# Kernel optimization log

Measured on AMD Instinct MI355X. Metric: run time of the kernel, lower is better.

The kernel has to match this reference:

```python
import jax, jax.numpy as jnp
import numpy as np

N, F, D, H, OUT = 4096, 64, 64, 4, 2
NEG_SLOPE = 0.2


def setup_inputs() -> dict:
    key = jax.random.key(0)
    ks = jax.random.split(key, 16)
    def p(k, shape, fan):
        return jax.random.normal(k, shape, dtype=jnp.float32) / np.float32(np.sqrt(fan))
    return {
        "x": jax.random.normal(ks[0], (N, F), dtype=jnp.float32),
        "W_enc": p(ks[1], (F, D), F), "b_enc": jnp.zeros((D,), jnp.float32),
        "W1": p(ks[2], (D, H * D), D), "a_src1": p(ks[3], (H, D), D),
        "a_dst1": p(ks[4], (H, D), D), "b1": jnp.zeros((D,), jnp.float32),
        "W2": p(ks[5], (D, H * D), D), "a_src2": p(ks[6], (H, D), D),
        "a_dst2": p(ks[7], (H, D), D), "b2": jnp.zeros((D,), jnp.float32),
        "W_act": p(ks[8], (D, OUT), D), "b_act": jnp.zeros((OUT,), jnp.float32),
        "W_cri": p(ks[9], (D, 1), D), "b_cri": jnp.zeros((1,), jnp.float32),
    }


def gat_conv(x, W, a_src, a_dst, b):
    # PyG GATConv, fully-connected graph (incl. self loops), concat=False (mean heads)
    n = x.shape[0]
    h = (x @ W).reshape(n, H, D)                      # [N,H,D]
    s_src = jnp.einsum('nhd,hd->nh', h, a_src)        # alpha_src per source node
    s_dst = jnp.einsum('nhd,hd->nh', h, a_dst)        # alpha_dst per target node
    # e[t,s,h] = leaky_relu(alpha_dst[t] + alpha_src[s]); softmax over sources s
    e = jax.nn.leaky_relu(s_dst[:, None, :] + s_src[None, :, :], NEG_SLOPE)
    attn = jax.nn.softmax(e, axis=1)                  # [N,N,H]
    out = jnp.einsum('tsh,shd->thd', attn, h)         # aggregate messages
    return out.mean(axis=1) + b                       # head mean + bias -> [N,D]


def reference(x, W_enc, b_enc, W1, a_src1, a_dst1, b1, W2, a_src2, a_dst2, b2,
              W_act, b_act, W_cri, b_cri):
    h = jax.nn.relu(x @ W_enc + b_enc)
    h = jax.nn.relu(gat_conv(h, W1, a_src1, a_dst1, b1))
    h = jax.nn.relu(gat_conv(h, W2, a_src2, a_dst2, b2))
    logits = jnp.clip(h @ W_act + b_act, -5.0, 5.0)
    logits = jnp.concatenate([logits[:, :1], jnp.abs(logits[:, 1:2])], axis=1)
    values = (h @ W_cri + b_cri).reshape(-1)
    return logits, values
```

## Files before the change

kernel.cpp:

```cpp
#include <hip/hip_runtime.h>


#define N 4096
#define D 64
#define H 4
#define HD 256
#define TS 66

#define AS(p, v) __hip_atomic_store((p), (v), __ATOMIC_RELAXED, __HIP_MEMORY_SCOPE_AGENT)
#define AL(p)    __hip_atomic_load((p), __ATOMIC_RELAXED, __HIP_MEMORY_SCOPE_AGENT)

__device__ __forceinline__ void fma4(float4& a, float s, const float4& b) {
  a.x = fmaf(s, b.x, a.x); a.y = fmaf(s, b.y, a.y);
  a.z = fmaf(s, b.z, a.z); a.w = fmaf(s, b.w, a.w);
}

__device__ __forceinline__ void proj_dev(const float (*xs)[64], int r0,
    const float* __restrict__ W, const float* __restrict__ asrc,
    const float* __restrict__ adst, float* __restrict__ h2,
    float* __restrict__ ssrc, float* __restrict__ sdst) {
  int tid = threadIdx.x;
  int lane6 = tid & 63;
  int c0 = lane6 * 4;
  int hh = lane6 >> 4;
  int rbase = (tid >> 6) * 2;
  float4 acc0 = make_float4(0.f, 0.f, 0.f, 0.f);
  float4 acc1 = make_float4(0.f, 0.f, 0.f, 0.f);
#pragma unroll
  for (int kq = 0; kq < 16; ++kq) {
    const float* Wk = W + kq * 4 * 256 + c0;
    float4 w0 = *(const float4*)(Wk);
    float4 w1 = *(const float4*)(Wk + 256);
    float4 w2 = *(const float4*)(Wk + 512);
    float4 w3 = *(const float4*)(Wk + 768);
    float4 x0 = *(const float4*)(&xs[rbase][kq * 4]);
    float4 x1 = *(const float4*)(&xs[rbase + 1][kq * 4]);
    fma4(acc0, x0.x, w0); fma4(acc0, x0.y, w1); fma4(acc0, x0.z, w2); fma4(acc0, x0.w, w3);
    fma4(acc1, x1.x, w0); fma4(acc1, x1.y, w1); fma4(acc1, x1.z, w2); fma4(acc1, x1.w, w3);
  }
  float4 av = *(const float4*)(asrc + c0);
  float4 bv = *(const float4*)(adst + c0);
#pragma unroll
  for (int r = 0; r < 2; ++r) {
    float4 a = (r == 0) ? acc0 : acc1;
    int row = r0 + rbase + r;
    *(float4*)(h2 + row * 256 + c0) = a;
    float ps = a.x * av.x + a.y * av.y + a.z * av.z + a.w * av.w;
    float pd = a.x * bv.x + a.y * bv.y + a.z * bv.z + a.w * bv.w;
#pragma unroll
    for (int off = 8; off > 0; off >>= 1) {
      ps += __shfl_down(ps, off);
      pd += __shfl_down(pd, off);
    }
    if ((lane6 & 15) == 0) {
      ssrc[hh * N + row] = ps;
      sdst[hh * N + row] = pd;
    }
  }
}

__global__ __launch_bounds__(256) void k_encproj(const float* __restrict__ x,
    const float* __restrict__ Wenc, const float* __restrict__ benc,
    const float* __restrict__ W, const float* __restrict__ asrc,
    const float* __restrict__ adst, float* __restrict__ h2,
    float* __restrict__ ssrc, float* __restrict__ sdst,
    int* __restrict__ sync) {
  __shared__ float xs[8][64];
  int tid = threadIdx.x;
  int r0 = blockIdx.x * 8;
  if (blockIdx.x == 0 && tid < 136) sync[tid] = 0;
  {
    int row = tid >> 5, c = (tid & 31) * 2;
    const float* xr = x + (r0 + row) * 64;
    float a0 = benc[c], a1 = benc[c + 1];
#pragma unroll
    for (int k = 0; k < 64; ++k) {
      float xv = xr[k];
      float2 w = *(const float2*)(Wenc + k * 64 + c);
      a0 = fmaf(xv, w.x, a0);
      a1 = fmaf(xv, w.y, a1);
    }
    xs[row][c] = fmaxf(a0, 0.f);
    xs[row][c + 1] = fmaxf(a1, 0.f);
  }
  __syncthreads();
  proj_dev(xs, r0, W, asrc, adst, h2, ssrc, sdst);
}

__global__ __launch_bounds__(256) void k_rank_f(const float* __restrict__ ssrc,
    int* __restrict__ rpart, int* __restrict__ cnt,
    float* __restrict__ srtv, int* __restrict__ srti) {
  __shared__ __align__(16) float vs[256];
  __shared__ int lastflag;
  int h = blockIdx.x >> 4, ig = blockIdx.x & 15, c = blockIdx.y;
  int tid = threadIdx.x;
  vs[tid] = ssrc[h * N + c * 256 + tid];
  __syncthreads();
  int i = ig * 256 + tid;
  float vi = ssrc[h * N + i];
  int jbase = c * 256;
  int rank = 0;
  const float4* vs4 = (const float4*)vs;
#pragma unroll 4
  for (int j4 = 0; j4 < 64; ++j4) {
    float4 q = vs4[j4];
    int jb = jbase + (j4 << 2);
    rank += (q.x < vi || (q.x == vi && jb < i));
    rank += (q.y < vi || (q.y == vi && jb + 1 < i));
    rank += (q.z < vi || (q.z == vi && jb + 2 < i));
    rank += (q.w < vi || (q.w == vi && jb + 3 < i));
  }
  AS(&rpart[(c * H + h) * N + i], rank);
  asm volatile("s_waitcnt vmcnt(0)" ::: "memory");
  __syncthreads();
  if (tid == 0) {
    int prev = __hip_atomic_fetch_add(&cnt[h * 16 + ig], 1,
                 __ATOMIC_RELAXED, __HIP_MEMORY_SCOPE_AGENT);
    lastflag = (prev == 15);
  }
  __syncthreads();
  if (lastflag) {
    int rk = 0;
#pragma unroll
    for (int cc = 0; cc < 16; ++cc) rk += AL(&rpart[(cc * H + h) * N + i]);
    srtv[h * N + rk] = vi;
    srti[h * N + rk] = i;
  }
}

__global__ __launch_bounds__(512) void k_s3off(const float* __restrict__ h2,
    const int* __restrict__ srti, const float* __restrict__ srtv,
    float* __restrict__ TA, float* __restrict__ TB, int* __restrict__ cnt,
    float* __restrict__ SA, float* __restrict__ PB,
    float* __restrict__ SufT, float* __restrict__ PreT) {
  __shared__ int pj[64];
  __shared__ float wa[64], wb[64];
  __shared__ float vt[64][66];
  __shared__ float segA[8][66], segB[8][66];
  __shared__ int lastflag;
  int h = blockIdx.x >> 6, c = blockIdx.x & 63;
  int tid = threadIdx.x, w = tid >> 6, lane = tid & 63;
  int j0 = c * 64;
  if (tid < 64) {
    int j = j0 + tid;
    pj[tid] = srti[h * N + j];
    float sv = srtv[h * N + j];
    float m1 = srtv[h * N + N - 1];
    wa[tid] = expf(sv - m1);
    wb[tid] = expf(0.2f * (sv - m1));
  }
  __syncthreads();
#pragma unroll
  for (int jj = 0; jj < 8; ++jj) {
    int j = jj * 8 + w;
    vt[j][lane] = h2[pj[j] * HD + h * 64 + lane];
  }
  __syncthreads();
  {
    float sA = 0.f, sB = 0.f;
#pragma unroll
    for (int jj = 0; jj < 8; ++jj) {
      int j = w * 8 + jj;
      float v = vt[j][lane];
      sA = fmaf(wa[j], v, sA);
      sB = fmaf(wb[j], v, sB);
    }
    segA[w][lane] = sA; segB[w][lane] = sB;
    if (lane == 0) {
      float swA = 0.f, swB = 0.f;
#pragma unroll
      for (int jj = 0; jj < 8; ++jj) { swA += wa[w * 8 + jj]; swB += wb[w * 8 + jj]; }
      segA[w][64] = swA; segB[w][64] = swB;
    }
  }
  __syncthreads();
  size_t base = (size_t)h * (N + 1);
  {
    float acc = 0.f;
    for (int w2 = w + 1; w2 < 8; ++w2) acc += segA[w2][lane];
#pragma unroll
    for (int jj = 7; jj >= 0; --jj) {
      int j = w * 8 + jj;
      acc = fmaf(wa[j], vt[j][lane], acc);
      SA[(base + j0 + j) * TS + lane] = acc;
    }
  }
  {
    float acc = 0.f;
    for (int w2 = 0; w2 < w; ++w2) acc += segB[w2][lane];
#pragma unroll
    for (int jj = 0; jj < 8; ++jj) {
      int j = w * 8 + jj;
      PB[(base + j0 + j) * TS + lane] = acc;
      acc = fmaf(wb[j], vt[j][lane], acc);
    }
  }
  if (lane == 0) {
    float a = 0.f;
    for (int w2 = w + 1; w2 < 8; ++w2) a += segA[w2][64];
#pragma unroll
    for (int jj = 7; jj >= 0; --jj) {
      int j = w * 8 + jj;
      a += wa[j];
      SA[(base + j0 + j) * TS + 64] = a;
    }
  }
  if (lane == 1) {
    float bsum = 0.f;
    for (int w2 = 0; w2 < w; ++w2) bsum += segB[w2][64];
#pragma unroll
    for (int jj = 0; jj < 8; ++jj) {
      int j = w * 8 + jj;
      PB[(base + j0 + j) * TS + 64] = bsum;
      bsum += wb[j];
    }
  }
  if (tid < 65) {
    float tA = 0.f, tB = 0.f;
#pragma unroll
    for (int w2 = 0; w2 < 8; ++w2) { tA += segA[w2][tid]; tB += segB[w2][tid]; }
    AS(&TA[(h * 64 + c) * TS + tid], tA);
    AS(&TB[(h * 64 + c) * TS + tid], tB);
  }
  asm volatile("s_waitcnt vmcnt(0)" ::: "memory");
  __syncthreads();
  if (tid == 0) {
    int prev = __hip_atomic_fetch_add(&cnt[h], 1,
                 __ATOMIC_RELAXED, __HIP_MEMORY_SCOPE_AGENT);
    lastflag = (prev == 63);
  }
  __syncthreads();
  if (!lastflag) return;
  __syncthreads();
#pragma unroll
  for (int it = 0; it < 9; ++it) {
    int idx = it * 512 + tid;
    if (idx < 64 * 65) {
      int cc = idx / 65, col = idx - cc * 65;
      vt[cc][col] = AL(&TA[(h * 64 + cc) * TS + col]);
    }
  }
  __syncthreads();
  if (tid < 65) {
    float acc = 0.f;
    SufT[(h * 65 + 64) * TS + tid] = 0.f;
    for (int cc = 63; cc >= 0; --cc) {
      SufT[(h * 65 + cc) * TS + tid] = acc;
      acc += vt[cc][tid];
    }
  }
  __syncthreads();
#pragma unroll
  for (int it = 0; it < 9; ++it) {
    int idx = it * 512 + tid;
    if (idx < 64 * 65) {
      int cc = idx / 65, col = idx - cc * 65;
      vt[cc][col] = AL(&TB[(h * 64 + cc) * TS + col]);
    }
  }
  __syncthreads();
  if (tid < 65) {
    float acc = 0.f;
    for (int cc = 0; cc < 64; ++cc) {
      PreT[(h * 65 + cc) * TS + tid] = acc;
      acc += vt[cc][tid];
    }
    PreT[(h * 65 + 64) * TS + tid] = acc;
    SA[(base + N) * TS + tid] = 0.f;
    PB[(base + N) * TS + tid] = 0.f;
  }
}

template <int MODE>
__device__ __forceinline__ void target_dev(int t0, int tid,
    const float* __restrict__ sdst, const float* __restrict__ srtv,
    const float* __restrict__ SA, const float* __restrict__ PB,
    const float* __restrict__ SufT, const float* __restrict__ PreT,
    const float* __restrict__ bias, float (*xsout)[64], const float (*bnd)[64],
    const float* __restrict__ Wact, const float* __restrict__ bact,
    const float* __restrict__ Wcri, const float* __restrict__ bcri,
    float* __restrict__ out, int ntask) {
  int lane = tid & 63;
  for (int task = 0; task < ntask; ++task) {
    int r = task * 4 + (tid >> 6);
    int t = t0 + r;
    float acc = 0.f;
#pragma unroll
    for (int h = 0; h < H; ++h) {
      const float* sv = srtv + h * N;
      float dst = sdst[h * N + t];
      float thr = -dst;
      float m1 = sv[N - 1];
      unsigned long long b1m = __ballot(bnd[h][lane] <= thr);
      int c1 = __popcll(b1m);
      int seg = c1 > 0 ? c1 - 1 : 0;
      unsigned long long b2m = __ballot(sv[seg * 64 + lane] <= thr);
      int k = seg * 64 + __popcll(b2m);
      int c = k >> 6;
      float u = dst + m1;
      float g = fmaxf(u, 0.2f * u);
      float wAt = expf(u - g);
      float wBt = expf(0.2f * u - g);
      const float* sa = SA + (size_t)(h * (N + 1) + k) * TS;
      const float* pb = PB + (size_t)(h * (N + 1) + k) * TS;
      const float* sf = SufT + (size_t)(h * 65 + c) * TS;
      const float* pr = PreT + (size_t)(h * 65 + c) * TS;
      float num = wAt * (sa[lane] + sf[lane]) + wBt * (pb[lane] + pr[lane]);
      float den = wAt * (sa[64] + sf[64]) + wBt * (pb[64] + pr[64]);
      acc += num / den;
    }
    float hv = fmaxf(acc * 0.25f + bias[lane], 0.f);
    if constexpr (MODE == 0) {
      xsout[r][lane] = hv;
    } else {
      float p0 = hv * Wact[lane * 2 + 0];
      float p1 = hv * Wact[lane * 2 + 1];
      float p2 = hv * Wcri[lane];
#pragma unroll
      for (int off = 32; off > 0; off >>= 1) {
        p0 += __shfl_down(p0, off);
        p1 += __shfl_down(p1, off);
        p2 += __shfl_down(p2, off);
      }
      if (lane == 0) {
        float l0 = fminf(fmaxf(p0 + bact[0], -5.f), 5.f);
        float l1 = fminf(fmaxf(p1 + bact[1], -5.f), 5.f);
        out[t * 2 + 0] = l0;
        out[t * 2 + 1] = fabsf(l1);
        out[2 * N + t] = p2 + bcri[0];
      }
    }
  }
}

__global__ __launch_bounds__(256) void k_targetproj(
    const float* __restrict__ sdst, const float* __restrict__ srtv,
    const float* __restrict__ SA, const float* __restrict__ PB,
    const float* __restrict__ SufT, const float* __restrict__ PreT,
    const float* __restrict__ bias,
    const float* __restrict__ W, const float* __restrict__ asrc,
    const float* __restrict__ adst, float* __restrict__ h2,
    float* __restrict__ ssrc2, float* __restrict__ sdst2) {
  __shared__ float xs[8][64];
  __shared__ float bnd[4][64];
  int tid = threadIdx.x;
  int r0 = blockIdx.x * 8;
  { int hh = tid >> 6, l = tid & 63; bnd[hh][l] = srtv[hh * N + l * 64]; }
  __syncthreads();
  target_dev<0>(r0, tid, sdst, srtv, SA, PB, SufT, PreT, bias, xs, bnd,
                nullptr, nullptr, nullptr, nullptr, nullptr, 2);
  __syncthreads();
  proj_dev(xs, r0, W, asrc, adst, h2, ssrc2, sdst2);
}

__global__ __launch_bounds__(256) void k_target2(
    const float* __restrict__ sdst, const float* __restrict__ srtv,
    const float* __restrict__ SA, const float* __restrict__ PB,
    const float* __restrict__ SufT, const float* __restrict__ PreT,
    const float* __restrict__ bias,
    const float* __restrict__ Wact, const float* __restrict__ bact,
    const float* __restrict__ Wcri, const float* __restrict__ bcri,
    float* __restrict__ out) {
  __shared__ float bnd[4][64];
  int tid = threadIdx.x;
  { int hh = tid >> 6, l = tid & 63; bnd[hh][l] = srtv[hh * N + l * 64]; }
  __syncthreads();
  target_dev<1>(blockIdx.x * 4, tid, sdst, srtv, SA, PB, SufT, PreT, bias,
                nullptr, bnd, Wact, bact, Wcri, bcri, out, 1);
}

extern "C" void kernel_launch(void* const* d_in, const int* in_sizes, int n_in,
                              void* d_out, int out_size, void* d_ws, size_t ws_size,
                              hipStream_t stream) {
    (void)in_sizes; (void)n_in; (void)out_size; (void)ws_size;
    const float* x     = (const float*)d_in[0];
    const float* W_enc = (const float*)d_in[1];
    const float* b_enc = (const float*)d_in[2];
    const float* W1    = (const float*)d_in[3];
    const float* as1   = (const float*)d_in[4];
    const float* ad1   = (const float*)d_in[5];
    const float* b1    = (const float*)d_in[6];
    const float* W2    = (const float*)d_in[7];
    const float* as2   = (const float*)d_in[8];
    const float* ad2   = (const float*)d_in[9];
    const float* b2    = (const float*)d_in[10];
    const float* W_act = (const float*)d_in[11];
    const float* b_act = (const float*)d_in[12];
    const float* W_cri = (const float*)d_in[13];
    const float* b_cri = (const float*)d_in[14];
    float* out = (float*)d_out;

    float* p = (float*)d_ws;
    float* h2    = p; p += N * HD;
    float* ssrc1 = p; p += H * N;
    float* sdst1 = p; p += H * N;
    float* ssrc2 = p; p += H * N;
    float* sdst2 = p; p += H * N;
    float* srtv  = p; p += H * N;
    int*   srti  = (int*)p; p += H * N;
    float* TA    = p; p += H * 64 * TS;
    float* TB    = p; p += H * 64 * TS;
    float* SufT  = p; p += H * 65 * TS;
    float* PreT  = p; p += H * 65 * TS;
    float* SA    = p; p += (size_t)H * (N + 1) * TS;
    float* PB    = p; p += (size_t)H * (N + 1) * TS;
    int*   rpart = (int*)p; p += 16 * H * N;
    int*   sync  = (int*)p; p += 256;

    int* rcnt1 = sync;
    int* scnt1 = sync + 64;
    int* rcnt2 = sync + 68;
    int* scnt2 = sync + 132;

    dim3 rgrid(64, 16);

    k_encproj<<<N / 8, 256, 0, stream>>>(x, W_enc, b_enc, W1, as1, ad1,
                                         h2, ssrc1, sdst1, sync);
    k_rank_f<<<rgrid, 256, 0, stream>>>(ssrc1, rpart, rcnt1, srtv, srti);
    k_s3off<<<256, 512, 0, stream>>>(h2, srti, srtv, TA, TB, scnt1, SA, PB, SufT, PreT);
    k_targetproj<<<N / 8, 256, 0, stream>>>(sdst1, srtv, SA, PB, SufT, PreT, b1,
                                            W2, as2, ad2, h2, ssrc2, sdst2);
    k_rank_f<<<rgrid, 256, 0, stream>>>(ssrc2, rpart, rcnt2, srtv, srti);
    k_s3off<<<256, 512, 0, stream>>>(h2, srti, srtv, TA, TB, scnt2, SA, PB, SufT, PreT);
    k_target2<<<N / 4, 256, 0, stream>>>(sdst2, srtv, SA, PB, SufT, PreT, b2,
                                         W_act, b_act, W_cri, b_cri, out);
}
```

Baseline: 100.7 us.

## Fuse rank sort into scan kernel with per-head grid barrier

```diff
diff --git a/kernel.cpp b/kernel.cpp
--- a/kernel.cpp
+++ b/kernel.cpp
@@ -68,7 +68,7 @@
   __shared__ float xs[8][64];
   int tid = threadIdx.x;
   int r0 = blockIdx.x * 8;
-  if (blockIdx.x == 0 && tid < 136) sync[tid] = 0;
+  if (blockIdx.x == 0 && tid < 16) sync[tid] = 0;
   {
     int row = tid >> 5, c = (tid & 31) * 2;
     const float* xr = x + (r0 + row) * 64;
@@ -87,65 +87,70 @@
   proj_dev(xs, r0, W, asrc, adst, h2, ssrc, sdst);
 }
 
-__global__ __launch_bounds__(256) void k_rank_f(const float* __restrict__ ssrc,
-    int* __restrict__ rpart, int* __restrict__ cnt,
-    float* __restrict__ srtv, int* __restrict__ srti) {
-  __shared__ __align__(16) float vs[256];
-  __shared__ int lastflag;
-  int h = blockIdx.x >> 4, ig = blockIdx.x & 15, c = blockIdx.y;
-  int tid = threadIdx.x;
-  vs[tid] = ssrc[h * N + c * 256 + tid];
-  __syncthreads();
-  int i = ig * 256 + tid;
-  float vi = ssrc[h * N + i];
-  int jbase = c * 256;
-  int rank = 0;
-  const float4* vs4 = (const float4*)vs;
-#pragma unroll 4
-  for (int j4 = 0; j4 < 64; ++j4) {
-    float4 q = vs4[j4];
-    int jb = jbase + (j4 << 2);
-    rank += (q.x < vi || (q.x == vi && jb < i));
-    rank += (q.y < vi || (q.y == vi && jb + 1 < i));
-    rank += (q.z < vi || (q.z == vi && jb + 2 < i));
-    rank += (q.w < vi || (q.w == vi && jb + 3 < i));
-  }
-  AS(&rpart[(c * H + h) * N + i], rank);
-  asm volatile("s_waitcnt vmcnt(0)" ::: "memory");
-  __syncthreads();
-  if (tid == 0) {
-    int prev = __hip_atomic_fetch_add(&cnt[h * 16 + ig], 1,
-                 __ATOMIC_RELAXED, __HIP_MEMORY_SCOPE_AGENT);
-    lastflag = (prev == 15);
-  }
-  __syncthreads();
-  if (lastflag) {
-    int rk = 0;
-#pragma unroll
-    for (int cc = 0; cc < 16; ++cc) rk += AL(&rpart[(cc * H + h) * N + i]);
-    srtv[h * N + rk] = vi;
-    srti[h * N + rk] = i;
-  }
-}
-
-__global__ __launch_bounds__(512) void k_s3off(const float* __restrict__ h2,
-    const int* __restrict__ srti, const float* __restrict__ srtv,
-    float* __restrict__ TA, float* __restrict__ TB, int* __restrict__ cnt,
+__global__ __launch_bounds__(512) void k_rankscan(const float* __restrict__ ssrc,
+    float* __restrict__ srtv, int* __restrict__ srti, int* __restrict__ rcnt,
+    const float* __restrict__ h2,
+    float* __restrict__ TA, float* __restrict__ TB, int* __restrict__ scnt,
     float* __restrict__ SA, float* __restrict__ PB,
     float* __restrict__ SufT, float* __restrict__ PreT) {
+  __shared__ __align__(16) float row[N];
+  __shared__ int rpartL[64][9];
   __shared__ int pj[64];
   __shared__ float wa[64], wb[64];
   __shared__ float vt[64][66];
   __shared__ float segA[8][66], segB[8][66];
   __shared__ int lastflag;
-  int h = blockIdx.x >> 6, c = blockIdx.x & 63;
-  int tid = threadIdx.x, w = tid >> 6, lane = tid & 63;
+  int b = blockIdx.x;
+  int h = b >> 6;
+  int tid = threadIdx.x, lane = tid & 63, w = tid >> 6;
+
+  {
+    int ig = b & 63;
+    const float4* src4 = (const float4*)(ssrc + h * N);
+    float4* row4 = (float4*)row;
+#pragma unroll
+    for (int it = 0; it < 2; ++it) row4[it * 512 + tid] = src4[it * 512 + tid];
+    __syncthreads();
+    int i = ig * 64 + lane;
+    float vi = row[i];
+    int rank = 0;
+    const float4* vs4 = (const float4*)row;
+    int jb0 = w * 512;
+#pragma unroll 4
+    for (int j4 = 0; j4 < 128; ++j4) {
+      float4 q = vs4[w * 128 + j4];
+      int jb = jb0 + (j4 << 2);
+      rank += (q.x < vi || (q.x == vi && jb < i));
+      rank += (q.y < vi || (q.y == vi && jb + 1 < i));
+      rank += (q.z < vi || (q.z == vi && jb + 2 < i));
+      rank += (q.w < vi || (q.w == vi && jb + 3 < i));
+    }
+    rpartL[lane][w] = rank;
+    __syncthreads();
+    if (tid < 64) {
+      int rk = 0;
+#pragma unroll
+      for (int ww = 0; ww < 8; ++ww) rk += rpartL[tid][ww];
+      int ii = ig * 64 + tid;
+      AS(&srtv[h * N + rk], row[ii]);
+      AS(&srti[h * N + rk], ii);
+    }
+    asm volatile("s_waitcnt vmcnt(0)" ::: "memory");
+    __syncthreads();
+    if (tid == 0) {
+      __hip_atomic_fetch_add(&rcnt[h], 1, __ATOMIC_RELAXED, __HIP_MEMORY_SCOPE_AGENT);
+      while (AL(&rcnt[h]) < 64) __builtin_amdgcn_s_sleep(2);
+    }
+    __syncthreads();
+  }
+
+  int c = b & 63;
   int j0 = c * 64;
   if (tid < 64) {
     int j = j0 + tid;
-    pj[tid] = srti[h * N + j];
-    float sv = srtv[h * N + j];
-    float m1 = srtv[h * N + N - 1];
+    pj[tid] = AL(&srti[h * N + j]);
+    float sv = AL(&srtv[h * N + j]);
+    float m1 = AL(&srtv[h * N + N - 1]);
     wa[tid] = expf(sv - m1);
     wb[tid] = expf(0.2f * (sv - m1));
   }
@@ -225,7 +230,7 @@
   asm volatile("s_waitcnt vmcnt(0)" ::: "memory");
   __syncthreads();
   if (tid == 0) {
-    int prev = __hip_atomic_fetch_add(&cnt[h], 1,
+    int prev = __hip_atomic_fetch_add(&scnt[h], 1,
                  __ATOMIC_RELAXED, __HIP_MEMORY_SCOPE_AGENT);
     lastflag = (prev == 63);
   }
@@ -404,24 +409,21 @@
     float* PreT  = p; p += H * 65 * TS;
     float* SA    = p; p += (size_t)H * (N + 1) * TS;
     float* PB    = p; p += (size_t)H * (N + 1) * TS;
-    int*   rpart = (int*)p; p += 16 * H * N;
-    int*   sync  = (int*)p; p += 256;
+    int*   sync  = (int*)p; p += 64;
 
     int* rcnt1 = sync;
-    int* scnt1 = sync + 64;
-    int* rcnt2 = sync + 68;
-    int* scnt2 = sync + 132;
-
-    dim3 rgrid(64, 16);
+    int* scnt1 = sync + 4;
+    int* rcnt2 = sync + 8;
+    int* scnt2 = sync + 12;
 
     k_encproj<<<N / 8, 256, 0, stream>>>(x, W_enc, b_enc, W1, as1, ad1,
                                          h2, ssrc1, sdst1, sync);
-    k_rank_f<<<rgrid, 256, 0, stream>>>(ssrc1, rpart, rcnt1, srtv, srti);
-    k_s3off<<<256, 512, 0, stream>>>(h2, srti, srtv, TA, TB, scnt1, SA, PB, SufT, PreT);
+    k_rankscan<<<256, 512, 0, stream>>>(ssrc1, srtv, srti, rcnt1,
+                                        h2, TA, TB, scnt1, SA, PB, SufT, PreT);
     k_targetproj<<<N / 8, 256, 0, stream>>>(sdst1, srtv, SA, PB, SufT, PreT, b1,
                                             W2, as2, ad2, h2, ssrc2, sdst2);
-    k_rank_f<<<rgrid, 256, 0, stream>>>(ssrc2, rpart, rcnt2, srtv, srti);
-    k_s3off<<<256, 512, 0, stream>>>(h2, srti, srtv, TA, TB, scnt2, SA, PB, SufT, PreT);
+    k_rankscan<<<256, 512, 0, stream>>>(ssrc2, srtv, srti, rcnt2,
+                                        h2, TA, TB, scnt2, SA, PB, SufT, PreT);
     k_target2<<<N / 4, 256, 0, stream>>>(sdst2, srtv, SA, PB, SufT, PreT, b2,
                                          W_act, b_act, W_cri, b_cri, out);
 }
```

Measured after the change: 112.6 us. 11.8% more time.

## Fuse rank sort and segment prefix kernels with in-kernel spin-wait barrier

Applied to the files above, without the earlier changes.

```diff
diff --git a/kernel.cpp b/kernel.cpp
--- a/kernel.cpp
+++ b/kernel.cpp
@@ -68,7 +68,7 @@
   __shared__ float xs[8][64];
   int tid = threadIdx.x;
   int r0 = blockIdx.x * 8;
-  if (blockIdx.x == 0 && tid < 136) sync[tid] = 0;
+  if (blockIdx.x == 0 && tid < 144) sync[tid] = 0;
   {
     int row = tid >> 5, c = (tid & 31) * 2;
     const float* xr = x + (r0 + row) * 64;
@@ -87,80 +87,89 @@
   proj_dev(xs, r0, W, asrc, adst, h2, ssrc, sdst);
 }
 
-__global__ __launch_bounds__(256) void k_rank_f(const float* __restrict__ ssrc,
-    int* __restrict__ rpart, int* __restrict__ cnt,
-    float* __restrict__ srtv, int* __restrict__ srti) {
-  __shared__ __align__(16) float vs[256];
-  __shared__ int lastflag;
-  int h = blockIdx.x >> 4, ig = blockIdx.x & 15, c = blockIdx.y;
-  int tid = threadIdx.x;
-  vs[tid] = ssrc[h * N + c * 256 + tid];
-  __syncthreads();
-  int i = ig * 256 + tid;
-  float vi = ssrc[h * N + i];
-  int jbase = c * 256;
-  int rank = 0;
-  const float4* vs4 = (const float4*)vs;
-#pragma unroll 4
-  for (int j4 = 0; j4 < 64; ++j4) {
-    float4 q = vs4[j4];
-    int jb = jbase + (j4 << 2);
-    rank += (q.x < vi || (q.x == vi && jb < i));
-    rank += (q.y < vi || (q.y == vi && jb + 1 < i));
-    rank += (q.z < vi || (q.z == vi && jb + 2 < i));
-    rank += (q.w < vi || (q.w == vi && jb + 3 < i));
-  }
-  AS(&rpart[(c * H + h) * N + i], rank);
-  asm volatile("s_waitcnt vmcnt(0)" ::: "memory");
-  __syncthreads();
-  if (tid == 0) {
-    int prev = __hip_atomic_fetch_add(&cnt[h * 16 + ig], 1,
-                 __ATOMIC_RELAXED, __HIP_MEMORY_SCOPE_AGENT);
-    lastflag = (prev == 15);
-  }
-  __syncthreads();
-  if (lastflag) {
-    int rk = 0;
-#pragma unroll
-    for (int cc = 0; cc < 16; ++cc) rk += AL(&rpart[(cc * H + h) * N + i]);
-    srtv[h * N + rk] = vi;
-    srti[h * N + rk] = i;
-  }
-}
-
-__global__ __launch_bounds__(512) void k_s3off(const float* __restrict__ h2,
-    const int* __restrict__ srti, const float* __restrict__ srtv,
-    float* __restrict__ TA, float* __restrict__ TB, int* __restrict__ cnt,
+__global__ __launch_bounds__(256, 4) void k_ranks3(const float* __restrict__ ssrc,
+    int* __restrict__ rpart, int* __restrict__ rcnt, int* __restrict__ done,
+    float* __restrict__ srtv, int* __restrict__ srti,
+    const float* __restrict__ h2,
+    float* __restrict__ TA, float* __restrict__ TB, int* __restrict__ scnt,
     float* __restrict__ SA, float* __restrict__ PB,
     float* __restrict__ SufT, float* __restrict__ PreT) {
+  __shared__ __align__(16) float vs[256];
+  __shared__ int flag;
   __shared__ int pj[64];
   __shared__ float wa[64], wb[64];
   __shared__ float vt[64][66];
-  __shared__ float segA[8][66], segB[8][66];
-  __shared__ int lastflag;
-  int h = blockIdx.x >> 6, c = blockIdx.x & 63;
-  int tid = threadIdx.x, w = tid >> 6, lane = tid & 63;
+  __shared__ float segA[4][66], segB[4][66];
+  int h = blockIdx.x >> 4, ig = blockIdx.x & 15, c16 = blockIdx.y;
+  int tid = threadIdx.x;
+
+  {
+    vs[tid] = ssrc[h * N + c16 * 256 + tid];
+    __syncthreads();
+    int i = ig * 256 + tid;
+    float vi = ssrc[h * N + i];
+    int jbase = c16 * 256;
+    int rank = 0;
+    const float4* vs4 = (const float4*)vs;
+#pragma unroll 4
+    for (int j4 = 0; j4 < 64; ++j4) {
+      float4 q = vs4[j4];
+      int jb = jbase + (j4 << 2);
+      rank += (q.x < vi || (q.x == vi && jb < i));
+      rank += (q.y < vi || (q.y == vi && jb + 1 < i));
+      rank += (q.z < vi || (q.z == vi && jb + 2 < i));
+      rank += (q.w < vi || (q.w == vi && jb + 3 < i));
+    }
+    AS(&rpart[(c16 * H + h) * N + i], rank);
+    asm volatile("s_waitcnt vmcnt(0)" ::: "memory");
+    __syncthreads();
+    if (tid == 0) {
+      int prev = __hip_atomic_fetch_add(&rcnt[h * 16 + ig], 1,
+                   __ATOMIC_RELAXED, __HIP_MEMORY_SCOPE_AGENT);
+      flag = (prev == 15);
+    }
+    __syncthreads();
+    if (flag) {
+      int rk = 0;
+#pragma unroll
+      for (int cc = 0; cc < 16; ++cc) rk += AL(&rpart[(cc * H + h) * N + i]);
+      AS(&srtv[h * N + rk], vi);
+      AS(&srti[h * N + rk], i);
+      asm volatile("s_waitcnt vmcnt(0)" ::: "memory");
+      __syncthreads();
+      if (tid == 0)
+        __hip_atomic_fetch_add(&done[h], 1, __ATOMIC_RELAXED, __HIP_MEMORY_SCOPE_AGENT);
+    }
+  }
+
+  if (c16 >= 4) return;
+  int c = ig * 4 + c16;
+  int w = tid >> 6, lane = tid & 63;
   int j0 = c * 64;
+  if (tid == 0) {
+    while (AL(&done[h]) < 16) __builtin_amdgcn_s_sleep(2);
+  }
+  __syncthreads();
   if (tid < 64) {
     int j = j0 + tid;
-    pj[tid] = srti[h * N + j];
-    float sv = srtv[h * N + j];
-    float m1 = srtv[h * N + N - 1];
+    pj[tid] = AL(&srti[h * N + j]);
+    float sv = AL(&srtv[h * N + j]);
+    float m1 = AL(&srtv[h * N + N - 1]);
     wa[tid] = expf(sv - m1);
     wb[tid] = expf(0.2f * (sv - m1));
   }
   __syncthreads();
 #pragma unroll
-  for (int jj = 0; jj < 8; ++jj) {
-    int j = jj * 8 + w;
+  for (int jj = 0; jj < 16; ++jj) {
+    int j = jj * 4 + w;
     vt[j][lane] = h2[pj[j] * HD + h * 64 + lane];
   }
   __syncthreads();
   {
     float sA = 0.f, sB = 0.f;
 #pragma unroll
-    for (int jj = 0; jj < 8; ++jj) {
-      int j = w * 8 + jj;
+    for (int jj = 0; jj < 16; ++jj) {
+      int j = w * 16 + jj;
       float v = vt[j][lane];
       sA = fmaf(wa[j], v, sA);
       sB = fmaf(wb[j], v, sB);
@@ -169,7 +178,7 @@
     if (lane == 0) {
       float swA = 0.f, swB = 0.f;
 #pragma unroll
-      for (int jj = 0; jj < 8; ++jj) { swA += wa[w * 8 + jj]; swB += wb[w * 8 + jj]; }
+      for (int jj = 0; jj < 16; ++jj) { swA += wa[w * 16 + jj]; swB += wb[w * 16 + jj]; }
       segA[w][64] = swA; segB[w][64] = swB;
     }
   }
@@ -177,10 +186,10 @@
   size_t base = (size_t)h * (N + 1);
   {
     float acc = 0.f;
-    for (int w2 = w + 1; w2 < 8; ++w2) acc += segA[w2][lane];
-#pragma unroll
-    for (int jj = 7; jj >= 0; --jj) {
-      int j = w * 8 + jj;
+    for (int w2 = w + 1; w2 < 4; ++w2) acc += segA[w2][lane];
+#pragma unroll
+    for (int jj = 15; jj >= 0; --jj) {
+      int j = w * 16 + jj;
       acc = fmaf(wa[j], vt[j][lane], acc);
       SA[(base + j0 + j) * TS + lane] = acc;
     }
@@ -189,18 +198,18 @@
     float acc = 0.f;
     for (int w2 = 0; w2 < w; ++w2) acc += segB[w2][lane];
 #pragma unroll
-    for (int jj = 0; jj < 8; ++jj) {
-      int j = w * 8 + jj;
+    for (int jj = 0; jj < 16; ++jj) {
+      int j = w * 16 + jj;
       PB[(base + j0 + j) * TS + lane] = acc;
       acc = fmaf(wb[j], vt[j][lane], acc);
     }
   }
   if (lane == 0) {
     float a = 0.f;
-    for (int w2 = w + 1; w2 < 8; ++w2) a += segA[w2][64];
-#pragma unroll
-    for (int jj = 7; jj >= 0; --jj) {
-      int j = w * 8 + jj;
+    for (int w2 = w + 1; w2 < 4; ++w2) a += segA[w2][64];
+#pragma unroll
+    for (int jj = 15; jj >= 0; --jj) {
+      int j = w * 16 + jj;
       a += wa[j];
       SA[(base + j0 + j) * TS + 64] = a;
     }
@@ -209,8 +218,8 @@
     float bsum = 0.f;
     for (int w2 = 0; w2 < w; ++w2) bsum += segB[w2][64];
 #pragma unroll
-    for (int jj = 0; jj < 8; ++jj) {
-      int j = w * 8 + jj;
+    for (int jj = 0; jj < 16; ++jj) {
+      int j = w * 16 + jj;
       PB[(base + j0 + j) * TS + 64] = bsum;
       bsum += wb[j];
     }
@@ -218,23 +227,23 @@
   if (tid < 65) {
     float tA = 0.f, tB = 0.f;
 #pragma unroll
-    for (int w2 = 0; w2 < 8; ++w2) { tA += segA[w2][tid]; tB += segB[w2][tid]; }
+    for (int w2 = 0; w2 < 4; ++w2) { tA += segA[w2][tid]; tB += segB[w2][tid]; }
     AS(&TA[(h * 64 + c) * TS + tid], tA);
     AS(&TB[(h * 64 + c) * TS + tid], tB);
   }
   asm volatile("s_waitcnt vmcnt(0)" ::: "memory");
   __syncthreads();
   if (tid == 0) {
-    int prev = __hip_atomic_fetch_add(&cnt[h], 1,
+    int prev = __hip_atomic_fetch_add(&scnt[h], 1,
                  __ATOMIC_RELAXED, __HIP_MEMORY_SCOPE_AGENT);
-    lastflag = (prev == 63);
-  }
-  __syncthreads();
-  if (!lastflag) return;
-  __syncthreads();
-#pragma unroll
-  for (int it = 0; it < 9; ++it) {
-    int idx = it * 512 + tid;
+    flag = (prev == 63);
+  }
+  __syncthreads();
+  if (!flag) return;
+  __syncthreads();
+#pragma unroll
+  for (int it = 0; it < 17; ++it) {
+    int idx = it * 256 + tid;
     if (idx < 64 * 65) {
       int cc = idx / 65, col = idx - cc * 65;
       vt[cc][col] = AL(&TA[(h * 64 + cc) * TS + col]);
@@ -251,8 +260,8 @@
   }
   __syncthreads();
 #pragma unroll
-  for (int it = 0; it < 9; ++it) {
-    int idx = it * 512 + tid;
+  for (int it = 0; it < 17; ++it) {
+    int idx = it * 256 + tid;
     if (idx < 64 * 65) {
       int cc = idx / 65, col = idx - cc * 65;
       vt[cc][col] = AL(&TB[(h * 64 + cc) * TS + col]);
@@ -408,20 +417,22 @@
     int*   sync  = (int*)p; p += 256;
 
     int* rcnt1 = sync;
-    int* scnt1 = sync + 64;
-    int* rcnt2 = sync + 68;
-    int* scnt2 = sync + 132;
+    int* done1 = sync + 64;
+    int* scnt1 = sync + 68;
+    int* rcnt2 = sync + 72;
+    int* done2 = sync + 136;
+    int* scnt2 = sync + 140;
 
     dim3 rgrid(64, 16);
 
     k_encproj<<<N / 8, 256, 0, stream>>>(x, W_enc, b_enc, W1, as1, ad1,
                                          h2, ssrc1, sdst1, sync);
-    k_rank_f<<<rgrid, 256, 0, stream>>>(ssrc1, rpart, rcnt1, srtv, srti);
-    k_s3off<<<256, 512, 0, stream>>>(h2, srti, srtv, TA, TB, scnt1, SA, PB, SufT, PreT);
+    k_ranks3<<<rgrid, 256, 0, stream>>>(ssrc1, rpart, rcnt1, done1, srtv, srti,
+                                        h2, TA, TB, scnt1, SA, PB, SufT, PreT);
     k_targetproj<<<N / 8, 256, 0, stream>>>(sdst1, srtv, SA, PB, SufT, PreT, b1,
                                             W2, as2, ad2, h2, ssrc2, sdst2);
-    k_rank_f<<<rgrid, 256, 0, stream>>>(ssrc2, rpart, rcnt2, srtv, srti);
-    k_s3off<<<256, 512, 0, stream>>>(h2, srti, srtv, TA, TB, scnt2, SA, PB, SufT, PreT);
+    k_ranks3<<<rgrid, 256, 0, stream>>>(ssrc2, rpart, rcnt2, done2, srtv, srti,
+                                        h2, TA, TB, scnt2, SA, PB, SufT, PreT);
     k_target2<<<N / 4, 256, 0, stream>>>(sdst2, srtv, SA, PB, SufT, PreT, b2,
                                          W_act, b_act, W_cri, b_cri, out);
 }
```

New measurement: 118.4 us. 1.18x slower.
